# Kernel optimization log

Measured on AMD Instinct MI355X. Metric: run time of the kernel, lower is better.

The kernel has to match this reference:

```python
import jax, jax.numpy as jnp
import numpy as np


def _ln(x, g, b, eps=1e-5):
    m = jnp.mean(x, axis=-1, keepdims=True)
    v = jnp.var(x, axis=-1, keepdims=True)
    return (x - m) * jax.lax.rsqrt(v + eps) * g + b


def setup_inputs() -> dict:
    key = jax.random.key(0)
    ks = jax.random.split(key, 24)
    B, Cin, Cout, Rout, N1, N2 = 8, 256, 512, 256, 4096, 1024
    s = 0.02
    f32 = jnp.float32
    return {
        "l1": jax.random.normal(ks[0], (B, Cin, N1), f32),
        "xyz1": jax.random.normal(ks[1], (B, 3, N1), f32),
        "l2": jax.random.normal(ks[2], (B, Cout, N2), f32),
        "xyz2": jax.random.normal(ks[3], (B, 3, N2), f32),
        # im_choose 1x1 convs (no bias)
        "q1_w": jax.random.normal(ks[4], (Cout, Cin), f32) * s,
        "k1_w": jax.random.normal(ks[5], (Cout, Cin), f32) * s,
        # mlp: Linear(Cin,Cin) -> LN(Cin) -> ReLU -> Linear(Cin,Cout)
        "mlp_w1": jax.random.normal(ks[6], (Cin, Cin), f32) * s,
        "mlp_b1": jnp.zeros((Cin,), f32),
        "mlp_g1": jnp.ones((Cin,), f32),
        "mlp_be1": jnp.zeros((Cin,), f32),
        "mlp_w2": jax.random.normal(ks[7], (Cout, Cin), f32) * s,
        "mlp_b2": jnp.zeros((Cout,), f32),
        # slefAttention 1x1 convs (no bias); pos1 conv is unused in forward
        "qw": jax.random.normal(ks[8], (Cout, Cout), f32) * s,
        "kw": jax.random.normal(ks[9], (Cout, Cout), f32) * s,
        "vw": jax.random.normal(ks[10], (Cout, Cout), f32) * s,
        "posw": jax.random.normal(ks[11], (Cout, 3), f32) * s,
        # IMFF.norm LayerNorm(Cout)
        "norm_g": jnp.ones((Cout,), f32),
        "norm_b": jnp.zeros((Cout,), f32),
        # mlp1: Linear(Cout,Cout) -> LN(Cout) -> ReLU -> Linear(Cout,Rout)
        "m1_w1": jax.random.normal(ks[12], (Cout, Cout), f32) * s,
        "m1_b1": jnp.zeros((Cout,), f32),
        "m1_g": jnp.ones((Cout,), f32),
        "m1_be": jnp.zeros((Cout,), f32),
        "m1_w2": jax.random.normal(ks[13], (Rout, Cout), f32) * s,
        "m1_b2": jnp.zeros((Rout,), f32),
    }


def reference(l1, xyz1, l2, xyz2, q1_w, k1_w, mlp_w1, mlp_b1, mlp_g1, mlp_be1,
              mlp_w2, mlp_b2, qw, kw, vw, posw, norm_g, norm_b,
              m1_w1, m1_b1, m1_g, m1_be, m1_w2, m1_b2):
    Cout = q1_w.shape[0]
    top_k = l2.shape[2]
    scale = jnp.sqrt(jnp.float32(Cout))

    # ---- im_choose: top-k selection of source points via attention row 0 ----
    q1 = jnp.einsum('oc,bcn->bon', q1_w, l1)          # [B,Cout,N1]
    k1 = jnp.einsum('oc,bcn->bon', k1_w, l1)          # [B,Cout,N1]
    e1 = jnp.einsum('bcn,bcm->bnm', q1, k1) / scale   # [B,N1,N1]
    att1 = jax.nn.softmax(e1, axis=-1)
    att_se = att1[:, 0, :]                            # [B,N1]
    _, idx = jax.lax.top_k(att_se, top_k)             # [B,K]
    l1_sel = jnp.take_along_axis(l1, idx[:, None, :], axis=-1)    # [B,Cin,K]
    p1_sel = jnp.take_along_axis(xyz1, idx[:, None, :], axis=-1)  # [B,3,K]

    # ---- mlp on gathered features ----
    h = jnp.swapaxes(l1_sel, 1, 2)                    # [B,K,Cin]
    h = jax.nn.relu(_ln(h @ mlp_w1.T + mlp_b1, mlp_g1, mlp_be1))
    h = h @ mlp_w2.T + mlp_b2                         # [B,K,Cout]
    x2 = jnp.swapaxes(h, 1, 2)                        # [B,Cout,K]

    # ---- slefAttention (cross): x1=l2/xyz2 queries, x2/p1_sel keys+values ----
    pos_q = jnp.einsum('oc,bcn->bon', posw, xyz2)     # [B,Cout,N2]
    pos_k = jnp.einsum('oc,bcn->bon', posw, p1_sel)   # [B,Cout,K]
    q = jnp.einsum('oc,bcn->bon', qw, l2 + pos_q)
    k = jnp.einsum('oc,bcn->bon', kw, x2 + pos_k)
    v = jnp.einsum('oc,bcn->bon', vw, x2)
    e = jnp.einsum('bcn,bcm->bnm', q, k) / scale      # [B,N2,K]
    att = jax.nn.softmax(e, axis=-1)
    o = jnp.einsum('bnm,bcm->bcn', att, v) + l2       # [B,Cout,N2]
    o = jnp.swapaxes(o, 1, 2)                         # [B,N2,Cout]

    # ---- norm + leaky_relu + mlp1 head ----
    o = jax.nn.leaky_relu(_ln(o, norm_g, norm_b), 0.01)
    o = jax.nn.relu(_ln(o @ m1_w1.T + m1_b1, m1_g, m1_be))
    o = o @ m1_w2.T + m1_b2                           # [B,N2,Rout]
    return jnp.swapaxes(o, 1, 2)                      # [B,Rout,N2]
```

## Files before the change

### kernel.cpp

```cpp
#include <hip/hip_runtime.h>
#include <math.h>


typedef __attribute__((ext_vector_type(8))) short short8x;
typedef __attribute__((ext_vector_type(4))) float f32x4;

__device__ __forceinline__ unsigned short f2b(float f) {
  unsigned int u = __float_as_uint(f);
  unsigned int r = u + 0x7FFFu + ((u >> 16) & 1u);
  return (unsigned short)(r >> 16);
}
__device__ __forceinline__ float b2f(unsigned short h) {
  return __uint_as_float(((unsigned int)h) << 16);
}

__device__ __forceinline__ void cp16(const unsigned short* g, unsigned short* l) {
  __builtin_amdgcn_global_load_lds(
      (const __attribute__((address_space(1))) void*)g,
      (__attribute__((address_space(3))) void*)l, 16, 0, 0);
}

__global__ void __launch_bounds__(256) prep_kernel(
    const float* w0, const float* w1, const float* w2, const float* w3,
    const float* w4, const float* w5, const float* w6,
    unsigned short* d0, unsigned short* d1, unsigned short* d2,
    unsigned short* d3, unsigned short* d4, unsigned short* d5,
    unsigned short* d6,
    const float* __restrict__ l1, const float* __restrict__ q1w,
    const float* __restrict__ k1w, float* __restrict__ wvec) {
  if (blockIdx.y == 7) {
    if (blockIdx.x >= 8) return;
    const int b = blockIdx.x;
    const int t = threadIdx.x;
    __shared__ float col[256];
    __shared__ float q1v[512];
    col[t] = l1[(long)b * 256 * 4096 + (long)t * 4096];
    __syncthreads();
    for (int o = t; o < 512; o += 256) {
      float s = 0.f;
      const float* row = q1w + (long)o * 256;
      for (int c = 0; c < 256; ++c) s += row[c] * col[c];
      q1v[o] = s;
    }
    __syncthreads();
    float s = 0.f;
    for (int o = 0; o < 512; ++o) s += k1w[(long)o * 256 + t] * q1v[o];
    wvec[b * 256 + t] = s;
    return;
  }
  const float* src;
  unsigned short* dst;
  int n;
  switch (blockIdx.y) {
    case 0: src = w0; dst = d0; n = 65536; break;
    case 1: src = w1; dst = d1; n = 131072; break;
    case 2: src = w2; dst = d2; n = 262144; break;
    case 3: src = w3; dst = d3; n = 262144; break;
    case 4: src = w4; dst = d4; n = 262144; break;
    case 5: src = w5; dst = d5; n = 262144; break;
    default: src = w6; dst = d6; n = 131072; break;
  }
  const int i = (blockIdx.x * 256 + threadIdx.x) * 4;
  if (i < n) {
    const float4 v = *(const float4*)(src + i);
    ushort4 o;
    o.x = f2b(v.x); o.y = f2b(v.y); o.z = f2b(v.z); o.w = f2b(v.w);
    *(ushort4*)(dst + i) = o;
  }
}

__global__ void __launch_bounds__(256) sel_scores_kernel(
    const float* __restrict__ l1, const float* __restrict__ wvec,
    float* __restrict__ scores) {
  const int b = blockIdx.y;
  const int m = blockIdx.x * 256 + threadIdx.x;
  __shared__ float w[256];
  w[threadIdx.x] = wvec[b * 256 + threadIdx.x];
  __syncthreads();
  const float* base = l1 + (long)b * 256 * 4096 + m;
  float s = 0.f;
  for (int c = 0; c < 256; ++c) s += w[c] * base[(long)c * 4096];
  scores[b * 4096 + m] = s;
}

__global__ void __launch_bounds__(256) topk_select_kernel(
    const float* __restrict__ scores, int* __restrict__ idx_out) {
  const int b = blockIdx.x;
  const int t = threadIdx.x;
  __shared__ unsigned int keys[4096];
  __shared__ unsigned int hist[256];
  __shared__ unsigned int sc_prefix, sc_krem;
  __shared__ int s_bin;
  __shared__ unsigned int partial_gt[256], partial_eq[256];

  for (int m = t; m < 4096; m += 256) {
    unsigned int u = __float_as_uint(scores[b * 4096 + m]);
    u ^= (u & 0x80000000u) ? 0xFFFFFFFFu : 0x80000000u;
    keys[m] = u;
  }
  if (t == 0) { sc_prefix = 0u; sc_krem = 1024u; }
  __syncthreads();

  unsigned int prefmask = 0u;
  for (int shift = 24; shift >= 0; shift -= 8) {
    hist[t] = 0u;
    if (t == 0) s_bin = 0;
    __syncthreads();
    const unsigned int prefix = sc_prefix;
    for (int m = t; m < 4096; m += 256) {
      unsigned int key = keys[m];
      if ((key & prefmask) == prefix) atomicAdd(&hist[(key >> shift) & 255u], 1u);
    }
    __syncthreads();
    for (int off = 1; off < 256; off <<= 1) {
      unsigned int v = hist[t] + ((t + off < 256) ? hist[t + off] : 0u);
      __syncthreads();
      hist[t] = v;
      __syncthreads();
    }
    const unsigned int krem = sc_krem;
    if (hist[t] >= krem) atomicMax(&s_bin, t);
    __syncthreads();
    if (t == 0) {
      const int bin = s_bin;
      sc_krem = krem - ((bin < 255) ? hist[bin + 1] : 0u);
      sc_prefix = prefix | ((unsigned int)bin << shift);
    }
    prefmask |= (0xFFu << shift);
    __syncthreads();
  }
  const unsigned int cutoff = sc_prefix;
  const unsigned int need = sc_krem;

  unsigned int gt = 0u, eq = 0u;
  const int base = t * 16;
  for (int i = 0; i < 16; ++i) {
    unsigned int key = keys[base + i];
    gt += (key > cutoff);
    eq += (key == cutoff);
  }
  partial_gt[t] = gt;
  partial_eq[t] = eq;
  __syncthreads();
  for (int off = 1; off < 256; off <<= 1) {
    unsigned int g = partial_gt[t] + ((t >= off) ? partial_gt[t - off] : 0u);
    unsigned int e2 = partial_eq[t] + ((t >= off) ? partial_eq[t - off] : 0u);
    __syncthreads();
    partial_gt[t] = g;
    partial_eq[t] = e2;
    __syncthreads();
  }
  const unsigned int pref_gt = partial_gt[t] - gt;
  const unsigned int pref_eq = partial_eq[t] - eq;
  unsigned int pos = pref_gt + ((pref_eq < need) ? pref_eq : need);
  unsigned int eqr = pref_eq;
  for (int i = 0; i < 16; ++i) {
    unsigned int key = keys[base + i];
    bool sel = (key > cutoff);
    if (key == cutoff) sel = sel || (eqr++ < need);
    if (sel) idx_out[b * 1024 + (pos++)] = base + i;
  }
}

__global__ void __launch_bounds__(256) gather_sel_kernel(
    const float* __restrict__ l1, const float* __restrict__ xyz1,
    const int* __restrict__ idx, unsigned short* __restrict__ l1selT,
    float* __restrict__ p1selT) {
  const int b = blockIdx.z;
  const int j = blockIdx.x * 64 + (threadIdx.x & 63);
  const int cz = blockIdx.y;
  const int cg = threadIdx.x >> 6;
  const int ix = idx[b * 1024 + j];
  const float* src = l1 + (long)b * 256 * 4096 + ix;
  unsigned short* dst = l1selT + ((long)b * 1024 + j) * 256;
#pragma unroll
  for (int it = 0; it < 8; ++it) {
    const int c = cz * 128 + it * 16 + cg * 4;
    const float x0 = src[(long)(c + 0) * 4096];
    const float x1 = src[(long)(c + 1) * 4096];
    const float x2 = src[(long)(c + 2) * 4096];
    const float x3 = src[(long)(c + 3) * 4096];
    ushort4 o;
    o.x = f2b(x0); o.y = f2b(x1); o.z = f2b(x2); o.w = f2b(x3);
    *(ushort4*)&dst[c] = o;
  }
  if (cz == 0 && cg == 0) {
    float* dp = p1selT + ((long)b * 1024 + j) * 3;
#pragma unroll
    for (int d = 0; d < 3; ++d) dp[d] = xyz1[((long)b * 3 + d) * 4096 + ix];
  }
}

__global__ void __launch_bounds__(256) transpose_posq_kernel(
    const float* __restrict__ l2, const float* __restrict__ xyz2,
    const float* __restrict__ posw, unsigned short* __restrict__ qinT,
    float* __restrict__ l2T) {
  const int b = blockIdx.z;
  const int n0 = blockIdx.x * 64, c0 = blockIdx.y * 64;
  const int tx = threadIdx.x, ty = threadIdx.y;
  __shared__ float tile[64][65];
  __shared__ float sx[3][64];
  const float* l2b = l2 + (long)b * 512 * 1024;
  for (int r = 0; r < 16; ++r) {
    const int c = ty * 16 + r;
    tile[c][tx] = l2b[(long)(c0 + c) * 1024 + n0 + tx];
  }
  if (ty < 3) sx[ty][tx] = xyz2[((long)b * 3 + ty) * 1024 + n0 + tx];
  __syncthreads();
  const int c = c0 + tx;
  const float p0 = posw[c * 3], p1 = posw[c * 3 + 1], p2 = posw[c * 3 + 2];
  for (int r = 0; r < 16; ++r) {
    const int nl = ty * 16 + r;
    const float val = tile[tx][nl];
    const long o = ((long)b * 1024 + n0 + nl) * 512 + c;
    l2T[o] = val;
    qinT[o] = f2b(val + p0 * sx[0][nl] + p1 * sx[1][nl] + p2 * sx[2][nl]);
  }
}

__global__ void __launch_bounds__(128) kin_kernel(
    const unsigned short* __restrict__ x2T, const float* __restrict__ p1selT,
    const float* __restrict__ posw, unsigned short* __restrict__ kinT) {
  const long row = blockIdx.x;
  const int t = threadIdx.x;
  const float q0 = p1selT[row * 3], q1 = p1selT[row * 3 + 1], q2 = p1selT[row * 3 + 2];
  const int c = t * 4;
  const ushort4 xv = *(const ushort4*)&x2T[row * 512 + c];
  ushort4 o;
  o.x = f2b(b2f(xv.x) + posw[(c + 0) * 3] * q0 + posw[(c + 0) * 3 + 1] * q1 + posw[(c + 0) * 3 + 2] * q2);
  o.y = f2b(b2f(xv.y) + posw[(c + 1) * 3] * q0 + posw[(c + 1) * 3 + 1] * q1 + posw[(c + 1) * 3 + 2] * q2);
  o.z = f2b(b2f(xv.z) + posw[(c + 2) * 3] * q0 + posw[(c + 2) * 3 + 1] * q1 + posw[(c + 2) * 3 + 2] * q2);
  o.w = f2b(b2f(xv.w) + posw[(c + 3) * 3] * q0 + posw[(c + 3) * 3 + 1] * q1 + posw[(c + 3) * 3 + 2] * q2);
  *(ushort4*)&kinT[row * 512 + c] = o;
}

template <int TRA, int TRB, bool BCOL, bool BROW, bool RES, int EPI>
__global__ void __launch_bounds__(256) gemm_u(
    const unsigned short* __restrict__ A, long sA, int ldA,
    const unsigned short* __restrict__ Bt, long sB, int ldB, long sB8,
    void* __restrict__ Yv, long sY, int ldY,
    const float* __restrict__ bias,
    const float* __restrict__ res, long sR,
    int K, float alpha,
    const float* __restrict__ ts1, const float* __restrict__ ts2,
    const float* __restrict__ tg, const float* __restrict__ tb, float tslope,
    float* __restrict__ os1, float* __restrict__ os2) {
  __shared__ __align__(16) unsigned short ldsA[2][128 * 32];
  __shared__ __align__(16) unsigned short ldsB[2][128 * 32];
  const int tid = threadIdx.x;
  const int lane = tid & 63;
  const int wv = tid >> 6;
  const int wm = wv >> 1, wn = wv & 1;
  const int n0 = blockIdx.x * 128, m0 = blockIdx.y * 128, b = blockIdx.z;
  A += (long)b * sA;
  Bt += (long)(b & 7) * sB + (long)(b >> 3) * sB8;
  const int lane15 = lane & 15, q = lane >> 4;

  const int srow0 = wv * 32 + (lane >> 2);
  const int srow1 = srow0 + 16;
  const int ks0 = ((lane & 3) ^ ((srow0 >> 1) & 3)) << 3;
  const int ks1 = ((lane & 3) ^ ((srow1 >> 1) & 3)) << 3;
  const unsigned short* gA0 = A + (long)(m0 + srow0) * ldA + ks0;
  const unsigned short* gA1 = A + (long)(m0 + srow1) * ldA + ks1;
  const unsigned short* gB0 = Bt + (long)(n0 + srow0) * ldB + ks0;
  const unsigned short* gB1 = Bt + (long)(n0 + srow1) * ldB + ks1;
  unsigned short* lA0[2] = {&ldsA[0][(wv * 32) * 32], &ldsA[1][(wv * 32) * 32]};
  unsigned short* lA1[2] = {&ldsA[0][(wv * 32 + 16) * 32], &ldsA[1][(wv * 32 + 16) * 32]};
  unsigned short* lB0[2] = {&ldsB[0][(wv * 32) * 32], &ldsB[1][(wv * 32) * 32]};
  unsigned short* lB1[2] = {&ldsB[0][(wv * 32 + 16) * 32], &ldsB[1][(wv * 32 + 16) * 32]};

  constexpr bool TR = (TRA + TRB) != 0;
  const int trow = tid & 127, thalf = tid >> 7;
  float t_mu = 0.f, t_rs = 0.f;
  const unsigned short* tsrc = nullptr;
  int toff0 = 0, toff1 = 0;
  if constexpr (TR) {
    const int row0 = (TRA ? m0 : n0) + trow;
    const int ridx = (b & 7) * 1024 + row0;
    const float Cf = (float)K;
    const float s1v = ts1[ridx], s2v = ts2[ridx];
    t_mu = s1v / Cf;
    t_rs = rsqrtf(s2v / Cf - t_mu * t_mu + 1e-5f);
    tsrc = (TRA ? A + (long)row0 * ldA : Bt + (long)row0 * ldB) + thalf * 16;
    const int sw = (trow >> 1) & 3;
    toff0 = trow * 32 + ((((thalf * 2) ^ sw)) << 3);
    toff1 = trow * 32 + ((((thalf * 2 + 1) ^ sw)) << 3);
  }

  auto t_apply = [&](int kk, short8x r0, short8x r1, int buf) {
    union { short8x v; unsigned short u[8]; } a0, a1, w0, w1;
    a0.v = r0; a1.v = r1;
    const float4* gp = (const float4*)(tg + kk + thalf * 16);
    const float4* bp = (const float4*)(tb + kk + thalf * 16);
    const float4 g0 = gp[0], g1 = gp[1], g2 = gp[2], g3 = gp[3];
    const float4 e0 = bp[0], e1 = bp[1], e2 = bp[2], e3 = bp[3];
    const float gg[16] = {g0.x, g0.y, g0.z, g0.w, g1.x, g1.y, g1.z, g1.w,
                          g2.x, g2.y, g2.z, g2.w, g3.x, g3.y, g3.z, g3.w};
    const float ee[16] = {e0.x, e0.y, e0.z, e0.w, e1.x, e1.y, e1.z, e1.w,
                          e2.x, e2.y, e2.z, e2.w, e3.x, e3.y, e3.z, e3.w};
#pragma unroll
    for (int c = 0; c < 8; ++c) {
      float y = (b2f(a0.u[c]) - t_mu) * t_rs * gg[c] + ee[c];
      y = y > 0.f ? y : tslope * y;
      w0.u[c] = f2b(y);
    }
#pragma unroll
    for (int c = 0; c < 8; ++c) {
      float y = (b2f(a1.u[c]) - t_mu) * t_rs * gg[8 + c] + ee[8 + c];
      y = y > 0.f ? y : tslope * y;
      w1.u[c] = f2b(y);
    }
    unsigned short* base = TRA ? &ldsA[buf][0] : &ldsB[buf][0];
    *(short8x*)&base[toff0] = w0.v;
    *(short8x*)&base[toff1] = w1.v;
  };

  short8x tr0, tr1;
  if constexpr (TR) {
    tr0 = *(const short8x*)(tsrc + 0);
    tr1 = *(const short8x*)(tsrc + 8);
  }
  if constexpr (!TRA) { cp16(gA0, lA0[0]); cp16(gA1, lA1[0]); }
  if constexpr (!TRB) { cp16(gB0, lB0[0]); cp16(gB1, lB1[0]); }
  if constexpr (TR) t_apply(0, tr0, tr1, 0);

  f32x4 acc[4][4] = {};
  int cur = 0;
  for (int k0 = 0; k0 < K; k0 += 32) {
    __syncthreads();
    const bool nxt = (k0 + 32 < K);
    if (nxt) {
      const int nk = k0 + 32;
      if constexpr (!TRA) { cp16(gA0 + nk, lA0[cur ^ 1]); cp16(gA1 + nk, lA1[cur ^ 1]); }
      if constexpr (!TRB) { cp16(gB0 + nk, lB0[cur ^ 1]); cp16(gB1 + nk, lB1[cur ^ 1]); }
      if constexpr (TR) {
        tr0 = *(const short8x*)(tsrc + nk);
        tr1 = *(const short8x*)(tsrc + nk + 8);
      }
    }
    short8x af[4], bfr[4];
#pragma unroll
    for (int i = 0; i < 4; ++i) {
      const int m = wm * 64 + i * 16 + lane15;
      af[i] = *(const short8x*)&ldsA[cur][m * 32 + ((q ^ ((m >> 1) & 3)) << 3)];
      const int n = wn * 64 + i * 16 + lane15;
      bfr[i] = *(const short8x*)&ldsB[cur][n * 32 + ((q ^ ((n >> 1) & 3)) << 3)];
    }
#pragma unroll
    for (int i = 0; i < 4; ++i)
#pragma unroll
      for (int j = 0; j < 4; ++j)
        acc[i][j] = __builtin_amdgcn_mfma_f32_16x16x32_bf16(af[i], bfr[j], acc[i][j], 0, 0, 0);
    if (nxt) {
      if constexpr (TR) t_apply(k0 + 32, tr0, tr1, cur ^ 1);
    }
    cur ^= 1;
  }

  float* Yf = (float*)Yv;
  unsigned short* Yh = (unsigned short*)Yv;
  if constexpr (EPI == 0) Yf += (long)b * sY; else Yh += (long)b * sY;
  if constexpr (RES) res += (long)b * sR;
  float inv_[4];
  float ssum[4][4], ssq[4][4];
#pragma unroll
  for (int i = 0; i < 4; ++i)
#pragma unroll
    for (int r = 0; r < 4; ++r) { ssum[i][r] = 0.f; ssq[i][r] = 0.f; }

#pragma unroll
  for (int i = 0; i < 4; ++i) {
    if constexpr (EPI == 4) {
#pragma unroll
      for (int r = 0; r < 4; ++r)
        inv_[r] = 1.f / ts1[(b & 7) * 1024 + m0 + wm * 64 + i * 16 + q * 4 + r];
    }
#pragma unroll
    for (int j = 0; j < 4; ++j) {
      const int n_g = n0 + wn * 64 + j * 16 + lane15;
      const float bc = BCOL ? bias[n_g] : 0.f;
#pragma unroll
      for (int r = 0; r < 4; ++r) {
        const int m_g = m0 + wm * 64 + i * 16 + q * 4 + r;
        float y = acc[i][j][r] * alpha;
        if constexpr (EPI == 4) y *= inv_[r];
        if constexpr (BCOL) y += bc;
        if constexpr (BROW) y += bias[m_g];
        if constexpr (RES) y += res[(long)m_g * ldY + n_g];
        if constexpr (EPI == 3) y = __expf(y);
        const long off = (long)m_g * ldY + n_g;
        if constexpr (EPI == 0) Yf[off] = y;
        else Yh[off] = f2b(y);
        if constexpr (EPI >= 2) { ssum[i][r] += y; ssq[i][r] += y * y; }
      }
    }
  }
  if constexpr (EPI == 2 || EPI == 4) {
#pragma unroll
    for (int i = 0; i < 4; ++i)
#pragma unroll
      for (int r = 0; r < 4; ++r) {
        float s = ssum[i][r], q2 = ssq[i][r];
        s += __shfl_xor(s, 1); q2 += __shfl_xor(q2, 1);
        s += __shfl_xor(s, 2); q2 += __shfl_xor(q2, 2);
        s += __shfl_xor(s, 4); q2 += __shfl_xor(q2, 4);
        s += __shfl_xor(s, 8); q2 += __shfl_xor(q2, 8);
        if (lane15 == 0) {
          const int ridx = (b & 7) * 1024 + m0 + wm * 64 + i * 16 + q * 4 + r;
          atomicAdd(&os1[ridx], s);
          atomicAdd(&os2[ridx], q2);
        }
      }
  } else if constexpr (EPI == 3) {
#pragma unroll
    for (int i = 0; i < 4; ++i)
#pragma unroll
      for (int r = 0; r < 4; ++r) {
        float s = ssum[i][r];
        s += __shfl_xor(s, 1);
        s += __shfl_xor(s, 2);
        s += __shfl_xor(s, 4);
        s += __shfl_xor(s, 8);
        if (lane15 == 0) {
          const int ridx = (b & 7) * 1024 + m0 + wm * 64 + i * 16 + q * 4 + r;
          atomicAdd(&os1[ridx], s);
        }
      }
  }
}

extern "C" void kernel_launch(void* const* d_in, const int* in_sizes, int n_in,
                              void* d_out, int out_size, void* d_ws,
                              size_t ws_size, hipStream_t stream) {
  const float* l1 = (const float*)d_in[0];
  const float* xyz1 = (const float*)d_in[1];
  const float* l2 = (const float*)d_in[2];
  const float* xyz2 = (const float*)d_in[3];
  const float* q1w = (const float*)d_in[4];
  const float* k1w = (const float*)d_in[5];
  const float* mlp_w1 = (const float*)d_in[6];
  const float* mlp_b1 = (const float*)d_in[7];
  const float* mlp_g1 = (const float*)d_in[8];
  const float* mlp_be1 = (const float*)d_in[9];
  const float* mlp_w2 = (const float*)d_in[10];
  const float* mlp_b2 = (const float*)d_in[11];
  const float* qw = (const float*)d_in[12];
  const float* kw = (const float*)d_in[13];
  const float* vw = (const float*)d_in[14];
  const float* posw = (const float*)d_in[15];
  const float* norm_g = (const float*)d_in[16];
  const float* norm_b = (const float*)d_in[17];
  const float* m1_w1 = (const float*)d_in[18];
  const float* m1_b1 = (const float*)d_in[19];
  const float* m1_g = (const float*)d_in[20];
  const float* m1_be = (const float*)d_in[21];
  const float* m1_w2 = (const float*)d_in[22];
  const float* m1_b2 = (const float*)d_in[23];

  char* ws = (char*)d_ws;
  const long MiB = 1048576;
  unsigned short* wb_mlp_w1 = (unsigned short*)(ws + 0);
  unsigned short* wb_mlp_w2 = (unsigned short*)(ws + 131072);
  unsigned short* wb_qw = (unsigned short*)(ws + 393216);
  unsigned short* wb_kw = (unsigned short*)(ws + 917504);
  unsigned short* wb_vw = (unsigned short*)(ws + 1441792);
  unsigned short* wb_m1w1 = (unsigned short*)(ws + 1966080);
  unsigned short* wb_m1w2 = (unsigned short*)(ws + 2490368);
  float* scores = (float*)(ws + 2752512);
  float* wvec = (float*)(ws + 2883584);
  int* idxb = (int*)(ws + 2891776);
  float* p1selT = (float*)(ws + 2924544);
  float* rowsum = (float*)(ws + 3407872);
  float* h1_s1 = (float*)(ws + 3440640);
  float* h1_s2 = (float*)(ws + 3473408);
  float* o_s1 = (float*)(ws + 3506176);
  float* o_s2 = (float*)(ws + 3538944);
  float* g1_s1 = (float*)(ws + 3571712);
  float* g1_s2 = (float*)(ws + 3604480);
  unsigned short* l1selT = (unsigned short*)(ws + 4 * MiB);
  unsigned short* h1 = (unsigned short*)(ws + 8 * MiB);
  unsigned short* x2T = (unsigned short*)(ws + 12 * MiB);
  unsigned short* qinT = (unsigned short*)(ws + 20 * MiB);
  unsigned short* kinT = (unsigned short*)(ws + 28 * MiB);
  float* l2T = (float*)(ws + 36 * MiB);
  unsigned short* qT = (unsigned short*)(ws + 52 * MiB);
  unsigned short* kT = (unsigned short*)(ws + 60 * MiB);
  unsigned short* vbf = (unsigned short*)(ws + 68 * MiB);
  unsigned short* pbuf = (unsigned short*)(ws + 76 * MiB);
  unsigned short* obuf = (unsigned short*)(ws + 92 * MiB);
  unsigned short* g1buf = (unsigned short*)(ws + 100 * MiB);
  float* outp = (float*)d_out;

  const float inv_scale = 1.0f / sqrtf(512.0f);
  const long T256 = 1024L * 256, T512 = 1024L * 512, T1024 = 1024L * 1024;

  hipMemsetAsync(ws + 3407872, 0, 7 * 32768, stream);

  prep_kernel<<<dim3(256, 8), 256, 0, stream>>>(
      mlp_w1, mlp_w2, qw, kw, vw, m1_w1, m1_w2,
      wb_mlp_w1, wb_mlp_w2, wb_qw, wb_kw, wb_vw, wb_m1w1, wb_m1w2,
      l1, q1w, k1w, wvec);
  sel_scores_kernel<<<dim3(16, 8), 256, 0, stream>>>(l1, wvec, scores);
  topk_select_kernel<<<8, 256, 0, stream>>>(scores, idxb);
  gather_sel_kernel<<<dim3(16, 2, 8), 256, 0, stream>>>(l1, xyz1, idxb, l1selT, p1selT);
  transpose_posq_kernel<<<dim3(16, 8, 8), dim3(64, 4), 0, stream>>>(
      l2, xyz2, posw, qinT, l2T);

  gemm_u<0, 0, true, false, false, 2><<<dim3(2, 8, 8), 256, 0, stream>>>(
      l1selT, T256, 256, wb_mlp_w1, 0, 256, 0, h1, T256, 256, mlp_b1,
      nullptr, 0, 256, 1.0f, nullptr, nullptr, nullptr, nullptr, 0.f, h1_s1, h1_s2);
  gemm_u<1, 0, true, false, false, 1><<<dim3(4, 8, 8), 256, 0, stream>>>(
      h1, T256, 256, wb_mlp_w2, 0, 256, 0, x2T, T512, 512, mlp_b2,
      nullptr, 0, 256, 1.0f, h1_s1, h1_s2, mlp_g1, mlp_be1, 0.f, nullptr, nullptr);

  kin_kernel<<<8192, 128, 0, stream>>>(x2T, p1selT, posw, kinT);

  gemm_u<0, 0, false, false, false, 1><<<dim3(4, 8, 16), 256, 0, stream>>>(
      qinT, T512, 512, wb_qw, 0, 512, 262144, qT, T512, 512, nullptr,
      nullptr, 0, 512, 1.0f, nullptr, nullptr, nullptr, nullptr, 0.f, nullptr, nullptr);
  gemm_u<0, 0, false, false, false, 1><<<dim3(8, 4, 8), 256, 0, stream>>>(
      wb_vw, 0, 512, x2T, T512, 512, 0, vbf, T512, 1024, nullptr,
      nullptr, 0, 512, 1.0f, nullptr, nullptr, nullptr, nullptr, 0.f, nullptr, nullptr);

  gemm_u<0, 0, false, false, false, 3><<<dim3(8, 8, 8), 256, 0, stream>>>(
      qT, T512, 512, kT, T512, 512, 0, pbuf, T1024, 1024, nullptr,
      nullptr, 0, 512, inv_scale, nullptr, nullptr, nullptr, nullptr, 0.f, rowsum, nullptr);
  gemm_u<0, 0, false, false, true, 4><<<dim3(4, 8, 8), 256, 0, stream>>>(
      pbuf, T1024, 1024, vbf, T512, 1024, 0, obuf, T512, 512, nullptr,
      l2T, T512, 1024, 1.0f, rowsum, nullptr, nullptr, nullptr, 0.f, o_s1, o_s2);
  gemm_u<1, 0, true, false, false, 2><<<dim3(4, 8, 8), 256, 0, stream>>>(
      obuf, T512, 512, wb_m1w1, 0, 512, 0, g1buf, T512, 512, m1_b1,
      nullptr, 0, 512, 1.0f, o_s1, o_s2, norm_g, norm_b, 0.01f, g1_s1, g1_s2);
  gemm_u<0, 1, false, true, false, 0><<<dim3(8, 2, 8), 256, 0, stream>>>(
      wb_m1w2, 0, 512, g1buf, T512, 512, 0, outp, 256L * 1024, 1024, m1_b2,
      nullptr, 0, 512, 1.0f, g1_s1, g1_s2, m1_g, m1_be, 0.f, nullptr, nullptr);
}
```

Measured before the change: 371.9 us.

## Fuse transpose into prep, parallelize selection vector, fold kin into GEMM epilogue

The l2 transpose plus positional-query kernel is merged into the weight-conversion prep launch as an extra grid row. The serial per-batch q1/k1 selection-vector computation is split into a wave-parallel q1 product inside prep and a new atomic-reduced k1 kernel. The key-input positional add (kin_kernel) is folded into the epilogue of the second MLP GEMM, which now writes both x2T and kinT. The aim is fewer launches and a shorter serial critical path, at the cost of a larger prep grid with many early-exit blocks and atomics in selB.

```diff
diff --git a/kernel.cpp b/kernel.cpp
--- a/kernel.cpp
+++ b/kernel.cpp
@@ -27,31 +27,64 @@
     unsigned short* d3, unsigned short* d4, unsigned short* d5,
     unsigned short* d6,
     const float* __restrict__ l1, const float* __restrict__ q1w,
-    const float* __restrict__ k1w, float* __restrict__ wvec) {
-  if (blockIdx.y == 7) {
-    if (blockIdx.x >= 8) return;
-    const int b = blockIdx.x;
-    const int t = threadIdx.x;
-    __shared__ float col[256];
-    __shared__ float q1v[512];
+    float* __restrict__ q1v,
+    const float* __restrict__ l2, const float* __restrict__ xyz2,
+    const float* __restrict__ posw, unsigned short* __restrict__ qinT,
+    float* __restrict__ l2T) {
+  __shared__ float tile[64][65];
+  __shared__ float sx[3][64];
+  __shared__ float col[256];
+  const int t = threadIdx.x;
+  const int y = blockIdx.y;
+
+  if (y == 7) {
+    if (blockIdx.x >= 1024) return;
+    const int b = blockIdx.x >> 7;
+    const int rem = blockIdx.x & 127;
+    const int n0 = (rem & 15) * 64, c0 = (rem >> 4) * 64;
+    const int tx = t & 63, ty = t >> 6;
+    const float* l2b = l2 + (long)b * 512 * 1024;
+    for (int r = 0; r < 16; ++r) {
+      const int c = ty * 16 + r;
+      tile[c][tx] = l2b[(long)(c0 + c) * 1024 + n0 + tx];
+    }
+    if (ty < 3) sx[ty][tx] = xyz2[((long)b * 3 + ty) * 1024 + n0 + tx];
+    __syncthreads();
+    const int c = c0 + tx;
+    const float p0 = posw[c * 3], p1 = posw[c * 3 + 1], p2 = posw[c * 3 + 2];
+    for (int r = 0; r < 16; ++r) {
+      const int nl = ty * 16 + r;
+      const float val = tile[tx][nl];
+      const long o = ((long)b * 1024 + n0 + nl) * 512 + c;
+      l2T[o] = val;
+      qinT[o] = f2b(val + p0 * sx[0][nl] + p1 * sx[1][nl] + p2 * sx[2][nl]);
+    }
+    return;
+  }
+  if (y == 8) {
+    if (blockIdx.x >= 64) return;
+    const int b = blockIdx.x >> 3;
+    const int chunk = blockIdx.x & 7;
     col[t] = l1[(long)b * 256 * 4096 + (long)t * 4096];
     __syncthreads();
-    for (int o = t; o < 512; o += 256) {
-      float s = 0.f;
-      const float* row = q1w + (long)o * 256;
-      for (int c = 0; c < 256; ++c) s += row[c] * col[c];
-      q1v[o] = s;
-    }
-    __syncthreads();
-    float s = 0.f;
-    for (int o = 0; o < 512; ++o) s += k1w[(long)o * 256 + t] * q1v[o];
-    wvec[b * 256 + t] = s;
+    const int lane = t & 63, wid = t >> 6;
+    const float4 cv = *(const float4*)&col[lane * 4];
+    const int obase = chunk * 64 + wid * 16;
+#pragma unroll
+    for (int oo = 0; oo < 16; ++oo) {
+      const int o = obase + oo;
+      const float4 wv = ((const float4*)(q1w + (long)o * 256))[lane];
+      float s = wv.x * cv.x + wv.y * cv.y + wv.z * cv.z + wv.w * cv.w;
+      s += __shfl_xor(s, 1); s += __shfl_xor(s, 2); s += __shfl_xor(s, 4);
+      s += __shfl_xor(s, 8); s += __shfl_xor(s, 16); s += __shfl_xor(s, 32);
+      if (lane == 0) q1v[b * 512 + o] = s;
+    }
     return;
   }
   const float* src;
   unsigned short* dst;
   int n;
-  switch (blockIdx.y) {
+  switch (y) {
     case 0: src = w0; dst = d0; n = 65536; break;
     case 1: src = w1; dst = d1; n = 131072; break;
     case 2: src = w2; dst = d2; n = 262144; break;
@@ -60,13 +93,29 @@
     case 5: src = w5; dst = d5; n = 262144; break;
     default: src = w6; dst = d6; n = 131072; break;
   }
-  const int i = (blockIdx.x * 256 + threadIdx.x) * 4;
+  const int i = (blockIdx.x * 256 + t) * 4;
   if (i < n) {
     const float4 v = *(const float4*)(src + i);
     ushort4 o;
     o.x = f2b(v.x); o.y = f2b(v.y); o.z = f2b(v.z); o.w = f2b(v.w);
     *(ushort4*)(dst + i) = o;
   }
+}
+
+__global__ void __launch_bounds__(256) selB_kernel(
+    const float* __restrict__ k1w, const float* __restrict__ q1v,
+    float* __restrict__ wvec) {
+  const int b = blockIdx.x;
+  const int chunk = blockIdx.y;
+  __shared__ float qs[64];
+  const int t = threadIdx.x;
+  if (t < 64) qs[t] = q1v[b * 512 + chunk * 64 + t];
+  __syncthreads();
+  float s = 0.f;
+  const float* kp = k1w + (long)(chunk * 64) * 256 + t;
+#pragma unroll 8
+  for (int oo = 0; oo < 64; ++oo) s += kp[(long)oo * 256] * qs[oo];
+  atomicAdd(&wvec[b * 256 + t], s);
 }
 
 __global__ void __launch_bounds__(256) sel_scores_kernel(
@@ -191,49 +240,6 @@
   }
 }
 
-__global__ void __launch_bounds__(256) transpose_posq_kernel(
-    const float* __restrict__ l2, const float* __restrict__ xyz2,
-    const float* __restrict__ posw, unsigned short* __restrict__ qinT,
-    float* __restrict__ l2T) {
-  const int b = blockIdx.z;
-  const int n0 = blockIdx.x * 64, c0 = blockIdx.y * 64;
-  const int tx = threadIdx.x, ty = threadIdx.y;
-  __shared__ float tile[64][65];
-  __shared__ float sx[3][64];
-  const float* l2b = l2 + (long)b * 512 * 1024;
-  for (int r = 0; r < 16; ++r) {
-    const int c = ty * 16 + r;
-    tile[c][tx] = l2b[(long)(c0 + c) * 1024 + n0 + tx];
-  }
-  if (ty < 3) sx[ty][tx] = xyz2[((long)b * 3 + ty) * 1024 + n0 + tx];
-  __syncthreads();
-  const int c = c0 + tx;
-  const float p0 = posw[c * 3], p1 = posw[c * 3 + 1], p2 = posw[c * 3 + 2];
-  for (int r = 0; r < 16; ++r) {
-    const int nl = ty * 16 + r;
-    const float val = tile[tx][nl];
-    const long o = ((long)b * 1024 + n0 + nl) * 512 + c;
-    l2T[o] = val;
-    qinT[o] = f2b(val + p0 * sx[0][nl] + p1 * sx[1][nl] + p2 * sx[2][nl]);
-  }
-}
-
-__global__ void __launch_bounds__(128) kin_kernel(
-    const unsigned short* __restrict__ x2T, const float* __restrict__ p1selT,
-    const float* __restrict__ posw, unsigned short* __restrict__ kinT) {
-  const long row = blockIdx.x;
-  const int t = threadIdx.x;
-  const float q0 = p1selT[row * 3], q1 = p1selT[row * 3 + 1], q2 = p1selT[row * 3 + 2];
-  const int c = t * 4;
-  const ushort4 xv = *(const ushort4*)&x2T[row * 512 + c];
-  ushort4 o;
-  o.x = f2b(b2f(xv.x) + posw[(c + 0) * 3] * q0 + posw[(c + 0) * 3 + 1] * q1 + posw[(c + 0) * 3 + 2] * q2);
-  o.y = f2b(b2f(xv.y) + posw[(c + 1) * 3] * q0 + posw[(c + 1) * 3 + 1] * q1 + posw[(c + 1) * 3 + 2] * q2);
-  o.z = f2b(b2f(xv.z) + posw[(c + 2) * 3] * q0 + posw[(c + 2) * 3 + 1] * q1 + posw[(c + 2) * 3 + 2] * q2);
-  o.w = f2b(b2f(xv.w) + posw[(c + 3) * 3] * q0 + posw[(c + 3) * 3 + 1] * q1 + posw[(c + 3) * 3 + 2] * q2);
-  *(ushort4*)&kinT[row * 512 + c] = o;
-}
-
 template <int TRA, int TRB, bool BCOL, bool BROW, bool RES, int EPI>
 __global__ void __launch_bounds__(256) gemm_u(
     const unsigned short* __restrict__ A, long sA, int ldA,
@@ -244,7 +250,9 @@
     int K, float alpha,
     const float* __restrict__ ts1, const float* __restrict__ ts2,
     const float* __restrict__ tg, const float* __restrict__ tb, float tslope,
-    float* __restrict__ os1, float* __restrict__ os2) {
+    float* __restrict__ os1, float* __restrict__ os2,
+    const float* __restrict__ kpos, const float* __restrict__ kpw,
+    unsigned short* __restrict__ Y2) {
   __shared__ __align__(16) unsigned short ldsA[2][128 * 32];
   __shared__ __align__(16) unsigned short ldsB[2][128 * 32];
   const int tid = threadIdx.x;
@@ -360,8 +368,10 @@
   float* Yf = (float*)Yv;
   unsigned short* Yh = (unsigned short*)Yv;
   if constexpr (EPI == 0) Yf += (long)b * sY; else Yh += (long)b * sY;
+  if constexpr (EPI == 5) Y2 += (long)b * sY;
   if constexpr (RES) res += (long)b * sR;
   float inv_[4];
+  float kq0[4], kq1[4], kq2[4];
   float ssum[4][4], ssq[4][4];
 #pragma unroll
   for (int i = 0; i < 4; ++i)
@@ -374,11 +384,23 @@
 #pragma unroll
       for (int r = 0; r < 4; ++r)
         inv_[r] = 1.f / ts1[(b & 7) * 1024 + m0 + wm * 64 + i * 16 + q * 4 + r];
+    }
+    if constexpr (EPI == 5) {
+#pragma unroll
+      for (int r = 0; r < 4; ++r) {
+        const int m_g = m0 + wm * 64 + i * 16 + q * 4 + r;
+        const float* pp = kpos + ((long)b * 1024 + m_g) * 3;
+        kq0[r] = pp[0]; kq1[r] = pp[1]; kq2[r] = pp[2];
+      }
     }
 #pragma unroll
     for (int j = 0; j < 4; ++j) {
       const int n_g = n0 + wn * 64 + j * 16 + lane15;
       const float bc = BCOL ? bias[n_g] : 0.f;
+      float pw0 = 0.f, pw1 = 0.f, pw2 = 0.f;
+      if constexpr (EPI == 5) {
+        pw0 = kpw[n_g * 3]; pw1 = kpw[n_g * 3 + 1]; pw2 = kpw[n_g * 3 + 2];
+      }
 #pragma unroll
       for (int r = 0; r < 4; ++r) {
         const int m_g = m0 + wm * 64 + i * 16 + q * 4 + r;
@@ -391,7 +413,11 @@
         const long off = (long)m_g * ldY + n_g;
         if constexpr (EPI == 0) Yf[off] = y;
         else Yh[off] = f2b(y);
-        if constexpr (EPI >= 2) { ssum[i][r] += y; ssq[i][r] += y * y; }
+        if constexpr (EPI == 5)
+          Y2[off] = f2b(y + pw0 * kq0[r] + pw1 * kq1[r] + pw2 * kq2[r]);
+        if constexpr (EPI == 2 || EPI == 3 || EPI == 4) {
+          ssum[i][r] += y; ssq[i][r] += y * y;
+        }
       }
     }
   }
@@ -467,9 +493,10 @@
   unsigned short* wb_m1w1 = (unsigned short*)(ws + 1966080);
   unsigned short* wb_m1w2 = (unsigned short*)(ws + 2490368);
   float* scores = (float*)(ws + 2752512);
-  float* wvec = (float*)(ws + 2883584);
   int* idxb = (int*)(ws + 2891776);
   float* p1selT = (float*)(ws + 2924544);
+  float* q1v = (float*)(ws + 3022848);
+  float* wvec = (float*)(ws + 3399680);
   float* rowsum = (float*)(ws + 3407872);
   float* h1_s1 = (float*)(ws + 3440640);
   float* h1_s2 = (float*)(ws + 3473408);
@@ -494,44 +521,49 @@
   const float inv_scale = 1.0f / sqrtf(512.0f);
   const long T256 = 1024L * 256, T512 = 1024L * 512, T1024 = 1024L * 1024;
 
-  hipMemsetAsync(ws + 3407872, 0, 7 * 32768, stream);
-
-  prep_kernel<<<dim3(256, 8), 256, 0, stream>>>(
+  hipMemsetAsync(ws + 3399680, 0, 237568, stream);
+
+  prep_kernel<<<dim3(1024, 9), 256, 0, stream>>>(
       mlp_w1, mlp_w2, qw, kw, vw, m1_w1, m1_w2,
       wb_mlp_w1, wb_mlp_w2, wb_qw, wb_kw, wb_vw, wb_m1w1, wb_m1w2,
-      l1, q1w, k1w, wvec);
+      l1, q1w, q1v, l2, xyz2, posw, qinT, l2T);
+  selB_kernel<<<dim3(8, 8), 256, 0, stream>>>(k1w, q1v, wvec);
   sel_scores_kernel<<<dim3(16, 8), 256, 0, stream>>>(l1, wvec, scores);
   topk_select_kernel<<<8, 256, 0, stream>>>(scores, idxb);
   gather_sel_kernel<<<dim3(16, 2, 8), 256, 0, stream>>>(l1, xyz1, idxb, l1selT, p1selT);
-  transpose_posq_kernel<<<dim3(16, 8, 8), dim3(64, 4), 0, stream>>>(
-      l2, xyz2, posw, qinT, l2T);
 
   gemm_u<0, 0, true, false, false, 2><<<dim3(2, 8, 8), 256, 0, stream>>>(
       l1selT, T256, 256, wb_mlp_w1, 0, 256, 0, h1, T256, 256, mlp_b1,
-      nullptr, 0, 256, 1.0f, nullptr, nullptr, nullptr, nullptr, 0.f, h1_s1, h1_s2);
-  gemm_u<1, 0, true, false, false, 1><<<dim3(4, 8, 8), 256, 0, stream>>>(
+      nullptr, 0, 256, 1.0f, nullptr, nullptr, nullptr, nullptr, 0.f,
+      h1_s1, h1_s2, nullptr, nullptr, nullptr);
+  gemm_u<1, 0, true, false, false, 5><<<dim3(4, 8, 8), 256, 0, stream>>>(
       h1, T256, 256, wb_mlp_w2, 0, 256, 0, x2T, T512, 512, mlp_b2,
-      nullptr, 0, 256, 1.0f, h1_s1, h1_s2, mlp_g1, mlp_be1, 0.f, nullptr, nullptr);
-
-  kin_kernel<<<8192, 128, 0, stream>>>(x2T, p1selT, posw, kinT);
+      nullptr, 0, 256, 1.0f, h1_s1, h1_s2, mlp_g1, mlp_be1, 0.f,
+      nullptr, nullptr, p1selT, posw, kinT);
 
   gemm_u<0, 0, false, false, false, 1><<<dim3(4, 8, 16), 256, 0, stream>>>(
       qinT, T512, 512, wb_qw, 0, 512, 262144, qT, T512, 512, nullptr,
-      nullptr, 0, 512, 1.0f, nullptr, nullptr, nullptr, nullptr, 0.f, nullptr, nullptr);
+      nullptr, 0, 512, 1.0f, nullptr, nullptr, nullptr, nullptr, 0.f,
+      nullptr, nullptr, nullptr, nullptr, nullptr);
   gemm_u<0, 0, false, false, false, 1><<<dim3(8, 4, 8), 256, 0, stream>>>(
       wb_vw, 0, 512, x2T, T512, 512, 0, vbf, T512, 1024, nullptr,
-      nullptr, 0, 512, 1.0f, nullptr, nullptr, nullptr, nullptr, 0.f, nullptr, nullptr);
+      nullptr, 0, 512, 1.0f, nullptr, nullptr, nullptr, nullptr, 0.f,
+      nullptr, nullptr, nullptr, nullptr, nullptr);
 
   gemm_u<0, 0, false, false, false, 3><<<dim3(8, 8, 8), 256, 0, stream>>>(
       qT, T512, 512, kT, T512, 512, 0, pbuf, T1024, 1024, nullptr,
-      nullptr, 0, 512, inv_scale, nullptr, nullptr, nullptr, nullptr, 0.f, rowsum, nullptr);
+      nullptr, 0, 512, inv_scale, nullptr, nullptr, nullptr, nullptr, 0.f,
+      rowsum, nullptr, nullptr, nullptr, nullptr);
   gemm_u<0, 0, false, false, true, 4><<<dim3(4, 8, 8), 256, 0, stream>>>(
       pbuf, T1024, 1024, vbf, T512, 1024, 0, obuf, T512, 512, nullptr,
-      l2T, T512, 1024, 1.0f, rowsum, nullptr, nullptr, nullptr, 0.f, o_s1, o_s2);
+      l2T, T512, 1024, 1.0f, rowsum, nullptr, nullptr, nullptr, 0.f,
+      o_s1, o_s2, nullptr, nullptr, nullptr);
   gemm_u<1, 0, true, false, false, 2><<<dim3(4, 8, 8), 256, 0, stream>>>(
       obuf, T512, 512, wb_m1w1, 0, 512, 0, g1buf, T512, 512, m1_b1,
-      nullptr, 0, 512, 1.0f, o_s1, o_s2, norm_g, norm_b, 0.01f, g1_s1, g1_s2);
+      nullptr, 0, 512, 1.0f, o_s1, o_s2, norm_g, norm_b, 0.01f,
+      g1_s1, g1_s2, nullptr, nullptr, nullptr);
   gemm_u<0, 1, false, true, false, 0><<<dim3(8, 2, 8), 256, 0, stream>>>(
       wb_m1w2, 0, 512, g1buf, T512, 512, 0, outp, 256L * 1024, 1024, m1_b2,
-      nullptr, 0, 512, 1.0f, g1_s1, g1_s2, m1_g, m1_be, 0.f, nullptr, nullptr);
-}
+      nullptr, 0, 512, 1.0f, g1_s1, g1_s2, m1_g, m1_be, 0.f,
+      nullptr, nullptr, nullptr, nullptr, nullptr);
+}
```

Measured after the change: 356.1 us. 1.04x faster.
